# Performance work log

Measured on AMD Instinct MI355X. Metric: run time of the kernel, lower is better.

The kernel has to match this reference:

```python
import jax, jax.numpy as jnp
import numpy as np
import math

DIM = 1024
NUM_HEADS = 16
HEAD_DIM = 64
SEQ_LEN = 2048
ATTN_SCALE = 0.12


def cosine_norm(x, eps=1e-12):
    # unit-normalize along last dim
    return x * jax.lax.rsqrt(jnp.sum(x * x, axis=-1, keepdims=True) + eps)


def rotary_tables(T, head_dim):
    dim_quarter = max(1, head_dim // 4)
    angular_freq = (1.0 / 1024.0) ** jnp.linspace(0.0, 1.0, dim_quarter, dtype=jnp.float32)
    angular_freq = jnp.concatenate([angular_freq, jnp.zeros(dim_quarter, dtype=jnp.float32)])  # [head_dim//2]
    t = jnp.arange(T, dtype=jnp.float32)
    theta = t[:, None] * angular_freq[None, :]  # [T, head_dim//2]
    return jnp.cos(theta), jnp.sin(theta)


def apply_rotary(x_BTHD, cos, sin):
    # cos/sin: [T, head_dim//2] -> broadcast [1, T, 1, head_dim//2]
    c = cos[None, :, None, :]
    s = sin[None, :, None, :]
    x1, x2 = jnp.split(x_BTHD, 2, axis=-1)
    y1 = x1 * c + x2 * s
    y2 = -x1 * s + x2 * c
    return jnp.concatenate([y1, y2], axis=-1)


def setup_inputs() -> dict:
    key = jax.random.key(0)
    ks = jax.random.split(key, 6)
    x = jax.random.normal(ks[0], (1, SEQ_LEN, DIM), dtype=jnp.float32)
    init_std = 0.02
    Wq = jax.random.normal(ks[1], (DIM, NUM_HEADS * HEAD_DIM), dtype=jnp.float32) * init_std
    Wk = jax.random.normal(ks[2], (DIM, NUM_HEADS * HEAD_DIM), dtype=jnp.float32) * init_std
    Wv = jax.random.normal(ks[3], (DIM, NUM_HEADS * HEAD_DIM), dtype=jnp.float32) * init_std
    Wo = jax.random.normal(ks[4], (NUM_HEADS * HEAD_DIM, DIM), dtype=jnp.float32) * init_std
    # Scale param: initialized as ones * (1/sqrt(dim)); use rand around that magnitude
    s_qk = jax.random.uniform(ks[5], (NUM_HEADS, HEAD_DIM), dtype=jnp.float32,
                              minval=0.5, maxval=1.5) * (1.0 / math.sqrt(DIM))
    return {"x": x, "Wq": Wq, "Wk": Wk, "Wv": Wv, "Wo": Wo, "s_qk": s_qk}


def reference(x, Wq, Wk, Wv, Wo, s_qk):
    B, T, _ = x.shape
    # projections
    q = (x @ Wq).reshape(B, T, NUM_HEADS, HEAD_DIM)
    k = (x @ Wk).reshape(B, T, NUM_HEADS, HEAD_DIM)
    v = (x @ Wv).reshape(B, T, NUM_HEADS, HEAD_DIM)
    # effective scale: s * (init/scale) with init=1, scale=1/sqrt(dim)
    s_eff = s_qk * math.sqrt(DIM)  # [H, D]
    q = cosine_norm(q) * s_eff[None, None, :, :]
    k = cosine_norm(k) * s_eff[None, None, :, :]
    cos, sin = rotary_tables(T, HEAD_DIM)
    q = apply_rotary(q, cos, sin)
    k = apply_rotary(k, cos, sin)
    # causal attention with fixed scale 0.12 (block_mask == causal)
    scores = jnp.einsum('bthd,bshd->bhts', q, k) * ATTN_SCALE  # [B,H,T,T]
    causal = jnp.tril(jnp.ones((T, T), dtype=bool))
    scores = jnp.where(causal[None, None, :, :], scores, jnp.float32(-1e30))
    attn = jax.nn.softmax(scores, axis=-1)
    y = jnp.einsum('bhts,bshd->bthd', attn, v)
    y = y.reshape(B, T, NUM_HEADS * HEAD_DIM)
    return y @ Wo
```

## Files before the change

kernel.cpp:

```cpp
#include <hip/hip_runtime.h>

typedef unsigned short u16;
typedef unsigned int u32;
typedef __attribute__((ext_vector_type(8))) short bf16x8;
typedef __attribute__((ext_vector_type(4))) float f32x4;

__device__ __forceinline__ u16 f2bf(float x) {
  unsigned u = __float_as_uint(x);
  u += 0x7fffu + ((u >> 16) & 1u);
  return (u16)(u >> 16);
}
__device__ __forceinline__ float bf2f(u16 z) {
  return __uint_as_float((u32)z << 16);
}
__device__ __forceinline__ u32 cvtpk(float lo, float hi) {
  u32 r;
  asm("v_cvt_pk_bf16_f32 %0, %1, %2" : "=v"(r) : "v"(lo), "v"(hi));
  return r;
}

__global__ __launch_bounds__(256) void prep(const float* __restrict__ x,
                                            const float* __restrict__ W0,
                                            const float* __restrict__ W1,
                                            const float* __restrict__ W2,
                                            const float* __restrict__ W3,
                                            u16* __restrict__ xb,
                                            u16* __restrict__ Wt,
                                            float2* __restrict__ rtab) {
  __shared__ alignas(16) u16 ls[64 * 72];
  int b = blockIdx.x;
  int tid = threadIdx.x;
  if (b < 2048) {
    int g = b * 256 + tid;
    int i = g * 4;
    float4 f = *(const float4*)(x + i);
    ushort4 o;
    o.x = f2bf(f.x); o.y = f2bf(f.y); o.z = f2bf(f.z); o.w = f2bf(f.w);
    *(ushort4*)(xb + i) = o;
    if (g < 2048 * 16) {
      int t = g >> 4, ii = g & 15;
      float fr = exp2f(-10.0f * (float)ii / 15.0f);
      float th = (float)t * fr;
      rtab[g] = make_float2(cosf(th), sinf(th));
    }
    return;
  }
  int bb = b - 2048;
  int z = bb >> 8;
  int rem = bb & 255;
  const float* W = (z == 0) ? W0 : (z == 1) ? W1 : (z == 2) ? W2 : W3;
  u16* o = Wt + (size_t)z * (1024u * 1024u);
  int kt = (rem >> 4) * 64, nt = (rem & 15) * 64;
  int r = tid >> 2, c0 = (tid & 3) * 16;
  const float* src = W + (size_t)(kt + r) * 1024 + nt + c0;
  u16 tmp[16];
#pragma unroll
  for (int c = 0; c < 16; c += 4) {
    float4 f = *(const float4*)(src + c);
    tmp[c + 0] = f2bf(f.x); tmp[c + 1] = f2bf(f.y);
    tmp[c + 2] = f2bf(f.z); tmp[c + 3] = f2bf(f.w);
  }
#pragma unroll
  for (int c = 0; c < 16; ++c) ls[r * 72 + c0 + c] = tmp[c];
  __syncthreads();
#pragma unroll
  for (int pass = 0; pass < 4; ++pass) {
    int n = pass * 16 + (tid >> 4);
    int kk = (tid & 15) * 4;
    ushort4 val;
    val.x = ls[(kk + 0) * 72 + n];
    val.y = ls[(kk + 1) * 72 + n];
    val.z = ls[(kk + 2) * 72 + n];
    val.w = ls[(kk + 3) * 72 + n];
    *(ushort4*)(o + (size_t)(nt + n) * 1024 + kt + kk) = val;
  }
}

#define GLD 40

__global__ __launch_bounds__(256) void gemm_qkv(const u16* __restrict__ A,
                                                const u16* __restrict__ Wt,
                                                u16* __restrict__ qb,
                                                u16* __restrict__ kb,
                                                u16* __restrict__ vt,
                                                const float* __restrict__ s_qk,
                                                const float2* __restrict__ rtab) {
  __shared__ alignas(16) u16 As[128 * GLD];
  __shared__ alignas(16) u16 Bs[128 * GLD];
  int z = blockIdx.z;
  const u16* B = Wt + (size_t)z * (1024u * 1024u);
  int tid = threadIdx.x;
  int bm = blockIdx.y * 128, bn = blockIdx.x * 128;
  int lane = tid & 63, w = tid >> 6;
  int wm = (w >> 1) * 64, wn = (w & 1) * 64;
  int m16 = lane & 15, q = lane >> 4;
  f32x4 acc[4][4] = {};
  int srow = tid >> 1, scol = (tid & 1) * 16;
  const u16* aptr = A + (size_t)(bm + srow) * 1024 + scol;
  const u16* bptr = B + (size_t)(bn + srow) * 1024 + scol;
  uint4 a0 = *(const uint4*)(aptr);
  uint4 a1 = *(const uint4*)(aptr + 8);
  uint4 b0 = *(const uint4*)(bptr);
  uint4 b1 = *(const uint4*)(bptr + 8);
  for (int k0 = 0; k0 < 1024; k0 += 32) {
    __syncthreads();
    *(uint4*)&As[srow * GLD + scol] = a0;
    *(uint4*)&As[srow * GLD + scol + 8] = a1;
    *(uint4*)&Bs[srow * GLD + scol] = b0;
    *(uint4*)&Bs[srow * GLD + scol + 8] = b1;
    uint4 na0, na1, nb0, nb1;
    if (k0 < 992) {
      na0 = *(const uint4*)(aptr + k0 + 32);
      na1 = *(const uint4*)(aptr + k0 + 40);
      nb0 = *(const uint4*)(bptr + k0 + 32);
      nb1 = *(const uint4*)(bptr + k0 + 40);
    }
    __syncthreads();
    bf16x8 af[4], bfr[4];
#pragma unroll
    for (int mt = 0; mt < 4; ++mt)
      af[mt] = *(const bf16x8*)&As[(wm + mt * 16 + m16) * GLD + q * 8];
#pragma unroll
    for (int nt = 0; nt < 4; ++nt)
      bfr[nt] = *(const bf16x8*)&Bs[(wn + nt * 16 + m16) * GLD + q * 8];
#pragma unroll
    for (int mt = 0; mt < 4; ++mt)
#pragma unroll
      for (int nt = 0; nt < 4; ++nt)
        acc[mt][nt] = __builtin_amdgcn_mfma_f32_16x16x32_bf16(af[mt], bfr[nt], acc[mt][nt], 0, 0, 0);
    if (k0 < 992) { a0 = na0; a1 = na1; b0 = nb0; b1 = nb1; }
  }
  int hh = (bn + wn) >> 6;
  if (z == 2) {
#pragma unroll
    for (int nt = 0; nt < 4; ++nt) {
      int n = bn + wn + nt * 16 + m16;
#pragma unroll
      for (int mt = 0; mt < 4; ++mt) {
        int t0 = bm + wm + mt * 16 + q * 4;
        ushort4 val;
        val.x = f2bf(acc[mt][nt][0]);
        val.y = f2bf(acc[mt][nt][1]);
        val.z = f2bf(acc[mt][nt][2]);
        val.w = f2bf(acc[mt][nt][3]);
        *(ushort4*)(vt + (size_t)n * 2048 + t0) = val;
      }
    }
  } else {
    u16* dst = z ? kb : qb;
    float se0 = s_qk[hh * 64 +  0 + m16] * 32.0f;
    float se1 = s_qk[hh * 64 + 16 + m16] * 32.0f;
    float se2 = s_qk[hh * 64 + 32 + m16] * 32.0f;
    float se3 = s_qk[hh * 64 + 48 + m16] * 32.0f;
#pragma unroll
    for (int mt = 0; mt < 4; ++mt)
#pragma unroll
      for (int r = 0; r < 4; ++r) {
        float ss = acc[mt][0][r] * acc[mt][0][r] + acc[mt][1][r] * acc[mt][1][r]
                 + acc[mt][2][r] * acc[mt][2][r] + acc[mt][3][r] * acc[mt][3][r];
        ss += __shfl_xor(ss, 1); ss += __shfl_xor(ss, 2);
        ss += __shfl_xor(ss, 4); ss += __shfl_xor(ss, 8);
        float inv = rsqrtf(ss + 1e-12f);
        int t = bm + wm + mt * 16 + q * 4 + r;
        float2 cs = rtab[t * 16 + m16];
        float x0 = acc[mt][0][r] * inv * se0;
        float x1 = acc[mt][1][r] * inv * se1;
        float x2 = acc[mt][2][r] * inv * se2;
        float x3 = acc[mt][3][r] * inv * se3;
        size_t off = (size_t)t * 1024 + hh * 64 + m16;
        dst[off]      = f2bf(x0 * cs.x + x2 * cs.y);
        dst[off + 16] = f2bf(x1);
        dst[off + 32] = f2bf(x2 * cs.x - x0 * cs.y);
        dst[off + 48] = f2bf(x3);
      }
  }
}

#define PLD 40
#define RPD 20
__global__ __launch_bounds__(256) void attn_flash(const u16* __restrict__ qb,
                                                  const u16* __restrict__ kb,
                                                  const u16* __restrict__ vt,
                                                  u16* __restrict__ yb) {
  __shared__ alignas(16) unsigned char smb[12 * 64 * RPD * 4 + 4 * 64 * 4];
  int h = blockIdx.x;
  int qt = 31 - blockIdx.y;
  int t0 = qt * 64;
  int tid = threadIdx.x;
  int lane = tid & 63, w = tid >> 6;
  int m16 = lane & 15, q = lane >> 4;
  u16* pw = (u16*)smb + w * 64 * PLD;
  bf16x8 qa[4][2];
#pragma unroll
  for (int qn = 0; qn < 4; ++qn) {
    const u16* qr = qb + (size_t)(t0 + qn * 16 + m16) * 1024 + h * 64;
    qa[qn][0] = *(const bf16x8*)(qr + q * 8);
    qa[qn][1] = *(const bf16x8*)(qr + 32 + q * 8);
  }
  int wk = w * 32;
  const u16* kbase = kb + (size_t)(wk + m16) * 1024 + h * 64 + q * 8;
  const u16* vbase = vt + (size_t)(h * 64 + m16) * 2048 + wk + q * 8;
  f32x4 Yacc[4][4] = {};
  float lsum[4] = {0.f, 0.f, 0.f, 0.f};
  int nkb = (qt + 2) >> 1;
  bf16x8 kfr[2][2];
#pragma unroll
  for (int kt = 0; kt < 2; ++kt) {
    kfr[kt][0] = *(const bf16x8*)(kbase + kt * 16384);
    kfr[kt][1] = *(const bf16x8*)(kbase + kt * 16384 + 32);
  }
  for (int kbi = 0; kbi < nkb; ++kbi) {
    int kb0 = kbi * 128;
    bf16x8 vfr[4];
#pragma unroll
    for (int nt = 0; nt < 4; ++nt)
      vfr[nt] = *(const bf16x8*)(vbase + (size_t)nt * 32768 + kb0);
    f32x4 ST[2][4] = {};
#pragma unroll
    for (int kt = 0; kt < 2; ++kt)
#pragma unroll
      for (int qn = 0; qn < 4; ++qn) {
        ST[kt][qn] = __builtin_amdgcn_mfma_f32_16x16x32_bf16(kfr[kt][0], qa[qn][0], ST[kt][qn], 0, 0, 0);
        ST[kt][qn] = __builtin_amdgcn_mfma_f32_16x16x32_bf16(kfr[kt][1], qa[qn][1], ST[kt][qn], 0, 0, 0);
      }
    bf16x8 kn[2][2];
    bool more = (kbi + 1 < nkb);
    if (more) {
      const u16* kp = kbase + (size_t)(kb0 + 128) * 1024;
#pragma unroll
      for (int kt = 0; kt < 2; ++kt) {
        kn[kt][0] = *(const bf16x8*)(kp + kt * 16384);
        kn[kt][1] = *(const bf16x8*)(kp + kt * 16384 + 32);
      }
    }
    bool last = (kbi == nkb - 1);
#pragma unroll
    for (int kt = 0; kt < 2; ++kt) {
      int keyb = kb0 + wk + kt * 16 + q * 4;
#pragma unroll
      for (int qn = 0; qn < 4; ++qn) {
        int qr_ = t0 + qn * 16 + m16;
        float p0 = __builtin_amdgcn_exp2f(ST[kt][qn][0] * 0.17312340490667562f);
        float p1 = __builtin_amdgcn_exp2f(ST[kt][qn][1] * 0.17312340490667562f);
        float p2 = __builtin_amdgcn_exp2f(ST[kt][qn][2] * 0.17312340490667562f);
        float p3 = __builtin_amdgcn_exp2f(ST[kt][qn][3] * 0.17312340490667562f);
        if (last) {
          p0 = (keyb + 0 <= qr_) ? p0 : 0.f;
          p1 = (keyb + 1 <= qr_) ? p1 : 0.f;
          p2 = (keyb + 2 <= qr_) ? p2 : 0.f;
          p3 = (keyb + 3 <= qr_) ? p3 : 0.f;
        }
        lsum[qn] += (p0 + p1) + (p2 + p3);
        uint2 pk2;
        pk2.x = cvtpk(p0, p1);
        pk2.y = cvtpk(p2, p3);
        *(uint2*)&pw[(qn * 16 + m16) * PLD + kt * 16 + q * 4] = pk2;
      }
    }
    bf16x8 pa[4];
#pragma unroll
    for (int qn = 0; qn < 4; ++qn)
      pa[qn] = *(const bf16x8*)&pw[(qn * 16 + m16) * PLD + q * 8];
#pragma unroll
    for (int qn = 0; qn < 4; ++qn)
#pragma unroll
      for (int nt = 0; nt < 4; ++nt)
        Yacc[qn][nt] = __builtin_amdgcn_mfma_f32_16x16x32_bf16(pa[qn], vfr[nt], Yacc[qn][nt], 0, 0, 0);
    if (more) {
      kfr[0][0] = kn[0][0]; kfr[0][1] = kn[0][1];
      kfr[1][0] = kn[1][0]; kfr[1][1] = kn[1][1];
    }
  }
#pragma unroll
  for (int qn = 0; qn < 4; ++qn) {
    lsum[qn] += __shfl_xor(lsum[qn], 16);
    lsum[qn] += __shfl_xor(lsum[qn], 32);
  }
  __syncthreads();
  float* Yr = (float*)smb;
  float* Lb = (float*)(smb + 12 * 64 * RPD * 4);
  if (q == 0) {
#pragma unroll
    for (int qn = 0; qn < 4; ++qn) Lb[w * 64 + qn * 16 + m16] = lsum[qn];
  }
#pragma unroll
  for (int qn = 0; qn < 4; ++qn) {
    if (qn != w) {
      int idx = w * 3 + (qn < w ? qn : qn - 1);
      float* dst = Yr + idx * 64 * RPD;
#pragma unroll
      for (int nt = 0; nt < 4; ++nt)
        *(f32x4*)&dst[(nt * 16 + m16) * RPD + q * 4] = Yacc[qn][nt];
    }
  }
  __syncthreads();
  float Lt[4];
#pragma unroll
  for (int r = 0; r < 4; ++r) {
    int row = w * 16 + q * 4 + r;
    Lt[r] = ((Lb[row] + Lb[64 + row]) + (Lb[128 + row] + Lb[192 + row]));
  }
#pragma unroll
  for (int nt = 0; nt < 4; ++nt) {
    f32x4 y = {0.f, 0.f, 0.f, 0.f};
#pragma unroll
    for (int qn = 0; qn < 4; ++qn)
      if (qn == w) y = Yacc[qn][nt];
#pragma unroll
    for (int wp = 0; wp < 4; ++wp) {
      if (wp != w) {
        int idx = wp * 3 + (w < wp ? w : w - 1);
        f32x4 o = *(const f32x4*)&Yr[idx * 64 * RPD + (nt * 16 + m16) * RPD + q * 4];
        y += o;
      }
    }
#pragma unroll
    for (int r = 0; r < 4; ++r) {
      int t = t0 + w * 16 + q * 4 + r;
      yb[(size_t)t * 1024 + h * 64 + nt * 16 + m16] =
          f2bf(y[r] * __builtin_amdgcn_rcpf(Lt[r]));
    }
  }
}

__global__ __launch_bounds__(256) void gemm_o(const u16* __restrict__ A,
                                              const u16* __restrict__ B,
                                              float* __restrict__ C) {
  __shared__ alignas(16) u16 As[128 * GLD];
  __shared__ alignas(16) u16 Bs[64 * GLD];
  int tid = threadIdx.x;
  int bm = blockIdx.y * 128, bn = blockIdx.x * 64;
  int lane = tid & 63, w = tid >> 6;
  int wm = w * 32;
  int m16 = lane & 15, q = lane >> 4;
  f32x4 acc[2][4] = {};
  int srA = tid >> 1, scA = (tid & 1) * 16;
  int srB = tid >> 2, scB = (tid & 3) * 8;
  const u16* aptr = A + (size_t)(bm + srA) * 1024 + scA;
  const u16* bptr = B + (size_t)(bn + srB) * 1024 + scB;
  uint4 a0 = *(const uint4*)(aptr);
  uint4 a1 = *(const uint4*)(aptr + 8);
  uint4 b0 = *(const uint4*)(bptr);
  for (int k0 = 0; k0 < 1024; k0 += 32) {
    __syncthreads();
    *(uint4*)&As[srA * GLD + scA] = a0;
    *(uint4*)&As[srA * GLD + scA + 8] = a1;
    *(uint4*)&Bs[srB * GLD + scB] = b0;
    uint4 na0, na1, nb0;
    if (k0 < 992) {
      na0 = *(const uint4*)(aptr + k0 + 32);
      na1 = *(const uint4*)(aptr + k0 + 40);
      nb0 = *(const uint4*)(bptr + k0 + 32);
    }
    __syncthreads();
    bf16x8 af[2], bfr[4];
#pragma unroll
    for (int mt = 0; mt < 2; ++mt)
      af[mt] = *(const bf16x8*)&As[(wm + mt * 16 + m16) * GLD + q * 8];
#pragma unroll
    for (int nt = 0; nt < 4; ++nt)
      bfr[nt] = *(const bf16x8*)&Bs[(nt * 16 + m16) * GLD + q * 8];
#pragma unroll
    for (int mt = 0; mt < 2; ++mt)
#pragma unroll
      for (int nt = 0; nt < 4; ++nt)
        acc[mt][nt] = __builtin_amdgcn_mfma_f32_16x16x32_bf16(af[mt], bfr[nt], acc[mt][nt], 0, 0, 0);
    if (k0 < 992) { a0 = na0; a1 = na1; b0 = nb0; }
  }
#pragma unroll
  for (int mt = 0; mt < 2; ++mt)
#pragma unroll
    for (int nt = 0; nt < 4; ++nt)
#pragma unroll
      for (int r = 0; r < 4; ++r) {
        int row = bm + wm + mt * 16 + q * 4 + r;
        int col = bn + nt * 16 + m16;
        C[(size_t)row * 1024 + col] = acc[mt][nt][r];
      }
}

extern "C" void kernel_launch(void* const* d_in, const int* in_sizes, int n_in,
                              void* d_out, int out_size, void* d_ws, size_t ws_size,
                              hipStream_t stream) {
  const float* x   = (const float*)d_in[0];
  const float* Wq  = (const float*)d_in[1];
  const float* Wk  = (const float*)d_in[2];
  const float* Wv  = (const float*)d_in[3];
  const float* Wo  = (const float*)d_in[4];
  const float* sqk = (const float*)d_in[5];
  float* out = (float*)d_out;
  char* ws = (char*)d_ws;

  u16*    xb   = (u16*)ws;
  u16*    Wt   = (u16*)(ws + ((size_t)4 << 20));
  float2* rtab = (float2*)(ws + ((size_t)12 << 20));
  u16*    qb16 = (u16*)(ws + ((size_t)16 << 20));
  u16*    kb16 = (u16*)(ws + ((size_t)20 << 20));
  u16*    vt16 = (u16*)(ws + ((size_t)24 << 20));
  u16*    yb   = (u16*)(ws + ((size_t)28 << 20));
  u16*    Wto  = Wt + (size_t)3 * 1024 * 1024;

  prep<<<3072, 256, 0, stream>>>(x, Wq, Wk, Wv, Wo, xb, Wt, rtab);
  gemm_qkv<<<dim3(8, 16, 3), 256, 0, stream>>>(xb, Wt, qb16, kb16, vt16, sqk, rtab);
  attn_flash<<<dim3(16, 32), 256, 0, stream>>>(qb16, kb16, vt16, yb);
  gemm_o<<<dim3(16, 16), 256, 0, stream>>>(yb, Wto, out);
}
```

Measured before the change: 145.6 us.

## Load GEMM tiles directly into LDS via global_load_lds, dropping register prefetch

Both projection GEMMs now fill their shared-memory tiles with direct global-to-LDS loads instead of loading into registers and storing to LDS. The padded LDS row stride is removed so each thread's 16-byte chunk maps contiguously. This saves VGPRs and LDS store instructions. It gives up the register double-buffer prefetch, so load latency is no longer overlapped with the previous tile's MFMAs, and the unpadded stride may cause LDS bank conflicts on fragment reads.

Result: slower. 150.1 us (+3.1%).

```diff
diff --git a/kernel.cpp b/kernel.cpp
--- a/kernel.cpp
+++ b/kernel.cpp
@@ -17,6 +17,11 @@
   u32 r;
   asm("v_cvt_pk_bf16_f32 %0, %1, %2" : "=v"(r) : "v"(lo), "v"(hi));
   return r;
+}
+__device__ __forceinline__ void gload16(const u16* g, u16* l) {
+  __builtin_amdgcn_global_load_lds(
+      (const __attribute__((address_space(1))) u32*)(const void*)g,
+      (__attribute__((address_space(3))) u32*)(void*)l, 16, 0, 0);
 }
 
 __global__ __launch_bounds__(256) void prep(const float* __restrict__ x,
@@ -76,8 +81,6 @@
   }
 }
 
-#define GLD 40
-
 __global__ __launch_bounds__(256) void gemm_qkv(const u16* __restrict__ A,
                                                 const u16* __restrict__ Wt,
                                                 u16* __restrict__ qb,
@@ -85,8 +88,8 @@
                                                 u16* __restrict__ vt,
                                                 const float* __restrict__ s_qk,
                                                 const float2* __restrict__ rtab) {
-  __shared__ alignas(16) u16 As[128 * GLD];
-  __shared__ alignas(16) u16 Bs[128 * GLD];
+  __shared__ alignas(16) u16 As[128 * 32];
+  __shared__ alignas(16) u16 Bs[128 * 32];
   int z = blockIdx.z;
   const u16* B = Wt + (size_t)z * (1024u * 1024u);
   int tid = threadIdx.x;
@@ -95,40 +98,30 @@
   int wm = (w >> 1) * 64, wn = (w & 1) * 64;
   int m16 = lane & 15, q = lane >> 4;
   f32x4 acc[4][4] = {};
-  int srow = tid >> 1, scol = (tid & 1) * 16;
+  int srow = tid >> 2, scol = (tid & 3) * 8;
   const u16* aptr = A + (size_t)(bm + srow) * 1024 + scol;
   const u16* bptr = B + (size_t)(bn + srow) * 1024 + scol;
-  uint4 a0 = *(const uint4*)(aptr);
-  uint4 a1 = *(const uint4*)(aptr + 8);
-  uint4 b0 = *(const uint4*)(bptr);
-  uint4 b1 = *(const uint4*)(bptr + 8);
+  u16* lA = As + tid * 8;
+  u16* lB = Bs + tid * 8;
   for (int k0 = 0; k0 < 1024; k0 += 32) {
     __syncthreads();
-    *(uint4*)&As[srow * GLD + scol] = a0;
-    *(uint4*)&As[srow * GLD + scol + 8] = a1;
-    *(uint4*)&Bs[srow * GLD + scol] = b0;
-    *(uint4*)&Bs[srow * GLD + scol + 8] = b1;
-    uint4 na0, na1, nb0, nb1;
-    if (k0 < 992) {
-      na0 = *(const uint4*)(aptr + k0 + 32);
-      na1 = *(const uint4*)(aptr + k0 + 40);
-      nb0 = *(const uint4*)(bptr + k0 + 32);
-      nb1 = *(const uint4*)(bptr + k0 + 40);
-    }
+    gload16(aptr + k0, lA);
+    gload16(aptr + k0 + (size_t)64 * 1024, lA + 64 * 32);
+    gload16(bptr + k0, lB);
+    gload16(bptr + k0 + (size_t)64 * 1024, lB + 64 * 32);
     __syncthreads();
     bf16x8 af[4], bfr[4];
 #pragma unroll
     for (int mt = 0; mt < 4; ++mt)
-      af[mt] = *(const bf16x8*)&As[(wm + mt * 16 + m16) * GLD + q * 8];
+      af[mt] = *(const bf16x8*)&As[(wm + mt * 16 + m16) * 32 + q * 8];
 #pragma unroll
     for (int nt = 0; nt < 4; ++nt)
-      bfr[nt] = *(const bf16x8*)&Bs[(wn + nt * 16 + m16) * GLD + q * 8];
+      bfr[nt] = *(const bf16x8*)&Bs[(wn + nt * 16 + m16) * 32 + q * 8];
 #pragma unroll
     for (int mt = 0; mt < 4; ++mt)
 #pragma unroll
       for (int nt = 0; nt < 4; ++nt)
         acc[mt][nt] = __builtin_amdgcn_mfma_f32_16x16x32_bf16(af[mt], bfr[nt], acc[mt][nt], 0, 0, 0);
-    if (k0 < 992) { a0 = na0; a1 = na1; b0 = nb0; b1 = nb1; }
   }
   int hh = (bn + wn) >> 6;
   if (z == 2) {
@@ -326,46 +319,37 @@
 __global__ __launch_bounds__(256) void gemm_o(const u16* __restrict__ A,
                                               const u16* __restrict__ B,
                                               float* __restrict__ C) {
-  __shared__ alignas(16) u16 As[128 * GLD];
-  __shared__ alignas(16) u16 Bs[64 * GLD];
+  __shared__ alignas(16) u16 As[128 * 32];
+  __shared__ alignas(16) u16 Bs[64 * 32];
   int tid = threadIdx.x;
   int bm = blockIdx.y * 128, bn = blockIdx.x * 64;
   int lane = tid & 63, w = tid >> 6;
   int wm = w * 32;
   int m16 = lane & 15, q = lane >> 4;
   f32x4 acc[2][4] = {};
-  int srA = tid >> 1, scA = (tid & 1) * 16;
-  int srB = tid >> 2, scB = (tid & 3) * 8;
-  const u16* aptr = A + (size_t)(bm + srA) * 1024 + scA;
-  const u16* bptr = B + (size_t)(bn + srB) * 1024 + scB;
-  uint4 a0 = *(const uint4*)(aptr);
-  uint4 a1 = *(const uint4*)(aptr + 8);
-  uint4 b0 = *(const uint4*)(bptr);
+  int srow = tid >> 2, scol = (tid & 3) * 8;
+  const u16* aptr = A + (size_t)(bm + srow) * 1024 + scol;
+  const u16* bptr = B + (size_t)(bn + srow) * 1024 + scol;
+  u16* lA = As + tid * 8;
+  u16* lB = Bs + tid * 8;
   for (int k0 = 0; k0 < 1024; k0 += 32) {
     __syncthreads();
-    *(uint4*)&As[srA * GLD + scA] = a0;
-    *(uint4*)&As[srA * GLD + scA + 8] = a1;
-    *(uint4*)&Bs[srB * GLD + scB] = b0;
-    uint4 na0, na1, nb0;
-    if (k0 < 992) {
-      na0 = *(const uint4*)(aptr + k0 + 32);
-      na1 = *(const uint4*)(aptr + k0 + 40);
-      nb0 = *(const uint4*)(bptr + k0 + 32);
-    }
+    gload16(aptr + k0, lA);
+    gload16(aptr + k0 + (size_t)64 * 1024, lA + 64 * 32);
+    gload16(bptr + k0, lB);
     __syncthreads();
     bf16x8 af[2], bfr[4];
 #pragma unroll
     for (int mt = 0; mt < 2; ++mt)
-      af[mt] = *(const bf16x8*)&As[(wm + mt * 16 + m16) * GLD + q * 8];
+      af[mt] = *(const bf16x8*)&As[(wm + mt * 16 + m16) * 32 + q * 8];
 #pragma unroll
     for (int nt = 0; nt < 4; ++nt)
-      bfr[nt] = *(const bf16x8*)&Bs[(nt * 16 + m16) * GLD + q * 8];
+      bfr[nt] = *(const bf16x8*)&Bs[(nt * 16 + m16) * 32 + q * 8];
 #pragma unroll
     for (int mt = 0; mt < 2; ++mt)
 #pragma unroll
       for (int nt = 0; nt < 4; ++nt)
         acc[mt][nt] = __builtin_amdgcn_mfma_f32_16x16x32_bf16(af[mt], bfr[nt], acc[mt][nt], 0, 0, 0);
-    if (k0 < 992) { a0 = na0; a1 = na1; b0 = nb0; }
   }
 #pragma unroll
   for (int mt = 0; mt < 2; ++mt)
```

## Halve attention query tile to 32 rows, doubling blocks and simplifying reduction

Applied to the files above, without the earlier changes.

The attention kernel now processes 32 query rows per block instead of 64 and launches twice as many blocks (16x64), giving more parallelism and better load balance across the causal triangle. The cross-wave reduction of partial outputs is rewritten so every wave writes its partial Y to shared memory and all threads sum four partials for their own rows. The software prefetch of the next K tile is dropped in favour of in-loop loads. In exchange, each K/V tile is loaded twice as often overall, and there is less MFMA work per loaded fragment.

New measurement: 157.1 us. 7.9% more time.

```diff
diff --git a/kernel.cpp b/kernel.cpp
--- a/kernel.cpp
+++ b/kernel.cpp
@@ -177,22 +177,22 @@
 }
 
 #define PLD 40
-#define RPD 20
+#define YSR 36
 __global__ __launch_bounds__(256) void attn_flash(const u16* __restrict__ qb,
                                                   const u16* __restrict__ kb,
                                                   const u16* __restrict__ vt,
                                                   u16* __restrict__ yb) {
-  __shared__ alignas(16) unsigned char smb[12 * 64 * RPD * 4 + 4 * 64 * 4];
+  __shared__ alignas(16) unsigned char smb[4 * 64 * YSR * 4 + 4 * 32 * 4];
   int h = blockIdx.x;
-  int qt = 31 - blockIdx.y;
-  int t0 = qt * 64;
+  int qt = 63 - blockIdx.y;
+  int t0 = qt * 32;
   int tid = threadIdx.x;
   int lane = tid & 63, w = tid >> 6;
   int m16 = lane & 15, q = lane >> 4;
-  u16* pw = (u16*)smb + w * 64 * PLD;
-  bf16x8 qa[4][2];
-#pragma unroll
-  for (int qn = 0; qn < 4; ++qn) {
+  u16* pw = (u16*)smb + w * 32 * PLD;
+  bf16x8 qa[2][2];
+#pragma unroll
+  for (int qn = 0; qn < 2; ++qn) {
     const u16* qr = qb + (size_t)(t0 + qn * 16 + m16) * 1024 + h * 64;
     qa[qn][0] = *(const bf16x8*)(qr + q * 8);
     qa[qn][1] = *(const bf16x8*)(qr + 32 + q * 8);
@@ -200,45 +200,36 @@
   int wk = w * 32;
   const u16* kbase = kb + (size_t)(wk + m16) * 1024 + h * 64 + q * 8;
   const u16* vbase = vt + (size_t)(h * 64 + m16) * 2048 + wk + q * 8;
-  f32x4 Yacc[4][4] = {};
-  float lsum[4] = {0.f, 0.f, 0.f, 0.f};
-  int nkb = (qt + 2) >> 1;
-  bf16x8 kfr[2][2];
-#pragma unroll
-  for (int kt = 0; kt < 2; ++kt) {
-    kfr[kt][0] = *(const bf16x8*)(kbase + kt * 16384);
-    kfr[kt][1] = *(const bf16x8*)(kbase + kt * 16384 + 32);
-  }
+  f32x4 Yacc[2][4] = {};
+  float lsum[2] = {0.f, 0.f};
+  int nkb = (qt + 4) >> 2;
   for (int kbi = 0; kbi < nkb; ++kbi) {
     int kb0 = kbi * 128;
+    bf16x8 kfr[2][2];
+#pragma unroll
+    for (int kt = 0; kt < 2; ++kt) {
+      const u16* kp = kbase + (size_t)kb0 * 1024 + kt * 16384;
+      kfr[kt][0] = *(const bf16x8*)kp;
+      kfr[kt][1] = *(const bf16x8*)(kp + 32);
+    }
     bf16x8 vfr[4];
 #pragma unroll
     for (int nt = 0; nt < 4; ++nt)
       vfr[nt] = *(const bf16x8*)(vbase + (size_t)nt * 32768 + kb0);
-    f32x4 ST[2][4] = {};
+    f32x4 ST[2][2] = {};
 #pragma unroll
     for (int kt = 0; kt < 2; ++kt)
 #pragma unroll
-      for (int qn = 0; qn < 4; ++qn) {
+      for (int qn = 0; qn < 2; ++qn) {
         ST[kt][qn] = __builtin_amdgcn_mfma_f32_16x16x32_bf16(kfr[kt][0], qa[qn][0], ST[kt][qn], 0, 0, 0);
         ST[kt][qn] = __builtin_amdgcn_mfma_f32_16x16x32_bf16(kfr[kt][1], qa[qn][1], ST[kt][qn], 0, 0, 0);
       }
-    bf16x8 kn[2][2];
-    bool more = (kbi + 1 < nkb);
-    if (more) {
-      const u16* kp = kbase + (size_t)(kb0 + 128) * 1024;
-#pragma unroll
-      for (int kt = 0; kt < 2; ++kt) {
-        kn[kt][0] = *(const bf16x8*)(kp + kt * 16384);
-        kn[kt][1] = *(const bf16x8*)(kp + kt * 16384 + 32);
-      }
-    }
     bool last = (kbi == nkb - 1);
 #pragma unroll
     for (int kt = 0; kt < 2; ++kt) {
       int keyb = kb0 + wk + kt * 16 + q * 4;
 #pragma unroll
-      for (int qn = 0; qn < 4; ++qn) {
+      for (int qn = 0; qn < 2; ++qn) {
         int qr_ = t0 + qn * 16 + m16;
         float p0 = __builtin_amdgcn_exp2f(ST[kt][qn][0] * 0.17312340490667562f);
         float p1 = __builtin_amdgcn_exp2f(ST[kt][qn][1] * 0.17312340490667562f);
@@ -257,69 +248,50 @@
         *(uint2*)&pw[(qn * 16 + m16) * PLD + kt * 16 + q * 4] = pk2;
       }
     }
-    bf16x8 pa[4];
-#pragma unroll
-    for (int qn = 0; qn < 4; ++qn)
+    bf16x8 pa[2];
+#pragma unroll
+    for (int qn = 0; qn < 2; ++qn)
       pa[qn] = *(const bf16x8*)&pw[(qn * 16 + m16) * PLD + q * 8];
 #pragma unroll
-    for (int qn = 0; qn < 4; ++qn)
+    for (int qn = 0; qn < 2; ++qn)
 #pragma unroll
       for (int nt = 0; nt < 4; ++nt)
         Yacc[qn][nt] = __builtin_amdgcn_mfma_f32_16x16x32_bf16(pa[qn], vfr[nt], Yacc[qn][nt], 0, 0, 0);
-    if (more) {
-      kfr[0][0] = kn[0][0]; kfr[0][1] = kn[0][1];
-      kfr[1][0] = kn[1][0]; kfr[1][1] = kn[1][1];
-    }
-  }
-#pragma unroll
-  for (int qn = 0; qn < 4; ++qn) {
+  }
+#pragma unroll
+  for (int qn = 0; qn < 2; ++qn) {
     lsum[qn] += __shfl_xor(lsum[qn], 16);
     lsum[qn] += __shfl_xor(lsum[qn], 32);
   }
   __syncthreads();
-  float* Yr = (float*)smb;
-  float* Lb = (float*)(smb + 12 * 64 * RPD * 4);
+  float* Ys = (float*)smb;
+  float* Lb = (float*)(smb + 4 * 64 * YSR * 4);
   if (q == 0) {
-#pragma unroll
-    for (int qn = 0; qn < 4; ++qn) Lb[w * 64 + qn * 16 + m16] = lsum[qn];
-  }
-#pragma unroll
-  for (int qn = 0; qn < 4; ++qn) {
-    if (qn != w) {
-      int idx = w * 3 + (qn < w ? qn : qn - 1);
-      float* dst = Yr + idx * 64 * RPD;
-#pragma unroll
-      for (int nt = 0; nt < 4; ++nt)
-        *(f32x4*)&dst[(nt * 16 + m16) * RPD + q * 4] = Yacc[qn][nt];
-    }
-  }
+    Lb[w * 32 + m16] = lsum[0];
+    Lb[w * 32 + 16 + m16] = lsum[1];
+  }
+#pragma unroll
+  for (int qn = 0; qn < 2; ++qn)
+#pragma unroll
+    for (int nt = 0; nt < 4; ++nt)
+      *(f32x4*)&Ys[(w * 64 + nt * 16 + m16) * YSR + qn * 16 + q * 4] = Yacc[qn][nt];
   __syncthreads();
+  int r0 = w * 8 + (q & 1) * 4;
   float Lt[4];
 #pragma unroll
-  for (int r = 0; r < 4; ++r) {
-    int row = w * 16 + q * 4 + r;
-    Lt[r] = ((Lb[row] + Lb[64 + row]) + (Lb[128 + row] + Lb[192 + row]));
-  }
-#pragma unroll
-  for (int nt = 0; nt < 4; ++nt) {
-    f32x4 y = {0.f, 0.f, 0.f, 0.f};
-#pragma unroll
-    for (int qn = 0; qn < 4; ++qn)
-      if (qn == w) y = Yacc[qn][nt];
-#pragma unroll
-    for (int wp = 0; wp < 4; ++wp) {
-      if (wp != w) {
-        int idx = wp * 3 + (w < wp ? w : w - 1);
-        f32x4 o = *(const f32x4*)&Yr[idx * 64 * RPD + (nt * 16 + m16) * RPD + q * 4];
-        y += o;
-      }
-    }
-#pragma unroll
-    for (int r = 0; r < 4; ++r) {
-      int t = t0 + w * 16 + q * 4 + r;
-      yb[(size_t)t * 1024 + h * 64 + nt * 16 + m16] =
-          f2bf(y[r] * __builtin_amdgcn_rcpf(Lt[r]));
-    }
+  for (int r = 0; r < 4; ++r)
+    Lt[r] = (Lb[r0 + r] + Lb[32 + r0 + r]) + (Lb[64 + r0 + r] + Lb[96 + r0 + r]);
+#pragma unroll
+  for (int p = 0; p < 2; ++p) {
+    int c = m16 + (q >> 1) * 16 + p * 32;
+    f32x4 s = {0.f, 0.f, 0.f, 0.f};
+#pragma unroll
+    for (int ws = 0; ws < 4; ++ws)
+      s += *(const f32x4*)&Ys[(ws * 64 + c) * YSR + r0];
+#pragma unroll
+    for (int r = 0; r < 4; ++r)
+      yb[(size_t)(t0 + r0 + r) * 1024 + h * 64 + c] =
+          f2bf(s[r] * __builtin_amdgcn_rcpf(Lt[r]));
   }
 }
 
@@ -402,6 +374,6 @@
 
   prep<<<3072, 256, 0, stream>>>(x, Wq, Wk, Wv, Wo, xb, Wt, rtab);
   gemm_qkv<<<dim3(8, 16, 3), 256, 0, stream>>>(xb, Wt, qb16, kb16, vt16, sqk, rtab);
-  attn_flash<<<dim3(16, 32), 256, 0, stream>>>(qb16, kb16, vt16, yb);
+  attn_flash<<<dim3(16, 64), 256, 0, stream>>>(qb16, kb16, vt16, yb);
   gemm_o<<<dim3(16, 16), 256, 0, stream>>>(yb, Wto, out);
 }
```
